# Kernel tuning notes

Measured on AMD Instinct MI355X. Metric: run time of the kernel, lower is better.

Reference implementation:

```python
import jax, jax.numpy as jnp
import numpy as np

NUM_ROUTES = 8
TEMPERATURE = 0.1
NEG_INF = -1e9
EPS = 1e-12  # F.normalize eps


def _l2_normalize(t):
    n = jnp.sqrt(jnp.sum(t * t, axis=-1, keepdims=True))
    return t / jnp.maximum(n, EPS)


def setup_inputs() -> dict:
    key = jax.random.key(0)
    ks = jax.random.split(key, 7)
    B, P1, D = 4, 2049, 1024
    s = 1.0 / np.sqrt(D)
    return {
        "x": jax.random.normal(ks[0], (B, P1, D), jnp.float32),
        "Wq": jax.random.normal(ks[1], (D, D), jnp.float32) * s,
        "bq": jax.random.normal(ks[2], (D,), jnp.float32) * 0.01,
        "Wk": jax.random.normal(ks[3], (D, D), jnp.float32) * s,
        "bk": jax.random.normal(ks[4], (D,), jnp.float32) * 0.01,
        "Wv": jax.random.normal(ks[5], (D, D), jnp.float32) * s,
        "bv": jax.random.normal(ks[6], (D,), jnp.float32) * 0.01,
    }


def reference(x, Wq, bq, Wk, bk, Wv, bv):
    x = x[:, 1:, :]  # skip_first=True
    B, P, D = x.shape
    q = _l2_normalize(x @ Wq.T + bq)
    k = _l2_normalize(x @ Wk.T + bk)
    v = x @ Wv.T + bv
    scores = jnp.einsum('bpd,bqd->bpq', q, k)  # [B,P,P]
    diag = jnp.eye(P, dtype=bool)
    scores = jnp.where(diag[None], NEG_INF, scores)
    topk_scores, routes = jax.lax.top_k(scores / TEMPERATURE, NUM_ROUTES)  # [B,P,K]
    weights = jax.nn.softmax(topk_scores, axis=-1)
    b_idx = jnp.arange(B)[:, None, None]
    v_gathered = v[b_idx, routes]  # [B,P,K,D]
    features = jnp.einsum('bpk,bpkd->bpd', weights, v_gathered)
    return routes, weights, features
```

## Files before the change

kernel.cpp:

```cpp
#include <hip/hip_runtime.h>
#include <hip/hip_bf16.h>
#include <math.h>

#define TEMP 0.1
#define NC 10

typedef float f4 __attribute__((ext_vector_type(4)));
typedef short s8v __attribute__((ext_vector_type(8)));
typedef int   i4v __attribute__((ext_vector_type(4)));
typedef _Float16 h8v __attribute__((ext_vector_type(8)));

__device__ inline short f2bf(float f) {
    __hip_bfloat16 h = __float2bfloat16(f);
    return *reinterpret_cast<short*>(&h);
}

__device__ __forceinline__ void g2l16(const void* g, void* l) {
    __builtin_amdgcn_global_load_lds(
        (const __attribute__((address_space(1))) void*)g,
        (__attribute__((address_space(3))) void*)l, 16, 0, 0);
}

__global__ __launch_bounds__(256) void prep_w(
    const float* __restrict__ Wq, const float* __restrict__ Wk,
    const float* __restrict__ Wv,
    signed char* __restrict__ Wql, signed char* __restrict__ Wkl,
    double* __restrict__ wqsc, double* __restrict__ wksc,
    short* __restrict__ Wvh)
{
    const int row = blockIdx.x, tid = threadIdx.x;
    const int which = blockIdx.y;
    if (which == 2) {
        const float4 v = ((const float4*)(Wv + (size_t)row * 1024))[tid];
        __align__(8) short h[4] = {f2bf(v.x), f2bf(v.y), f2bf(v.z), f2bf(v.w)};
        *(short4*)&Wvh[(size_t)row * 1024 + tid * 4] = *(short4*)h;
        return;
    }
    const float* src = which ? Wk : Wq;
    signed char* limbs = which ? Wkl : Wql;
    double* scale = which ? wksc : wqsc;
    const long plane_stride = 1024L * 1024;

    const float4 v = ((const float4*)(src + (size_t)row * 1024))[tid];
    float m = fmaxf(fmaxf(fabsf(v.x), fabsf(v.y)), fmaxf(fabsf(v.z), fabsf(v.w)));
#pragma unroll
    for (int off = 32; off > 0; off >>= 1) m = fmaxf(m, __shfl_down(m, off));
    __shared__ float wmax[4];
    __shared__ int ssig;
    if ((tid & 63) == 0) wmax[tid >> 6] = m;
    __syncthreads();
    if (tid == 0) {
        float rm = fmaxf(fmaxf(wmax[0], wmax[1]), fmaxf(wmax[2], wmax[3]));
        int sig = (rm > 0.f) ? (29 - ilogbf(rm)) : 0;
        ssig = sig;
        scale[row] = ldexp(1.0, -sig);
    }
    __syncthreads();
    const double s2 = ldexp(1.0, ssig);
    float xs[4] = {v.x, v.y, v.z, v.w};
    signed char out[4][4];
#pragma unroll
    for (int e = 0; e < 4; ++e) {
        long X = __double2ll_rn((double)xs[e] * s2);
#pragma unroll
        for (int l = 0; l < 3; ++l) {
            int d = (int)(((X + 128) & 255) - 128);
            out[l][e] = (signed char)d;
            X = (X - d) >> 8;
        }
        out[3][e] = (signed char)X;
    }
#pragma unroll
    for (int l = 0; l < 4; ++l)
        *(char4*)&limbs[(size_t)l * plane_stride + (size_t)row * 1024 + tid * 4] =
            *(char4*)&out[l][0];
}

__global__ __launch_bounds__(256) void prep_x(
    const float* __restrict__ src, signed char* __restrict__ limbs,
    long plane_stride, double* __restrict__ scale,
    short* __restrict__ hi)
{
    const int row = blockIdx.x, tid = threadIdx.x;
    const float4 v = ((const float4*)(src + (size_t)row * 1024))[tid];
    float m = fmaxf(fmaxf(fabsf(v.x), fabsf(v.y)), fmaxf(fabsf(v.z), fabsf(v.w)));
#pragma unroll
    for (int off = 32; off > 0; off >>= 1) m = fmaxf(m, __shfl_down(m, off));
    __shared__ float wmax[4];
    __shared__ int ssig;
    if ((tid & 63) == 0) wmax[tid >> 6] = m;
    __syncthreads();
    if (tid == 0) {
        float rm = fmaxf(fmaxf(wmax[0], wmax[1]), fmaxf(wmax[2], wmax[3]));
        int sig = (rm > 0.f) ? (29 - ilogbf(rm)) : 0;
        ssig = sig;
        scale[row] = ldexp(1.0, -sig);
    }
    __syncthreads();
    const double s2 = ldexp(1.0, ssig);
    float xs[4] = {v.x, v.y, v.z, v.w};
    signed char out[4][4];
    __align__(8) short h[4];
#pragma unroll
    for (int e = 0; e < 4; ++e) {
        long X = __double2ll_rn((double)xs[e] * s2);
#pragma unroll
        for (int lmb = 0; lmb < 3; ++lmb) {
            int d = (int)(((X + 128) & 255) - 128);
            out[lmb][e] = (signed char)d;
            X = (X - d) >> 8;
        }
        out[3][e] = (signed char)X;
        h[e] = f2bf(xs[e]);
    }
#pragma unroll
    for (int lmb = 0; lmb < 4; ++lmb)
        *(char4*)&limbs[(size_t)lmb * plane_stride + (size_t)row * 1024 + tid * 4] =
            *(char4*)&out[lmb][0];
    *(short4*)&hi[(size_t)row * 1024 + tid * 4] = *(short4*)h;
}

__global__ __launch_bounds__(256, 2) void gemm_i8qk(
    const signed char* __restrict__ Xl,
    const signed char* __restrict__ Wql,
    const signed char* __restrict__ Wkl,
    const double* __restrict__ xsc,
    const double* __restrict__ wqsc, const double* __restrict__ wksc,
    const float* __restrict__ bq, const float* __restrict__ bk,
    float* __restrict__ Qf, float* __restrict__ Kf)
{
    const int K = 1024, N = 1024;
    const long MK = 2048L * 1024, NK = 1024L * 1024;

    __shared__ __align__(16) signed char Asm[4][64][64];
    __shared__ __align__(16) signed char Bqm[4][64][64];
    __shared__ __align__(16) signed char Bkm[4][64][64];

    const int tid  = threadIdx.x;
    const int lane = tid & 63, wave = tid >> 6;
    const int wm = wave >> 1, wn = wave & 1;
    const int quad = lane >> 4, l16 = lane & 15;
    const int m0 = blockIdx.y * 64, n0 = blockIdx.x * 64;

    const int srow = tid >> 2;
    const int cswz = ((tid & 3) ^ ((srow >> 1) & 3));
    const signed char* ap  = Xl  + (size_t)(m0 + srow) * K + cswz * 16;
    const signed char* bqp = Wql + (size_t)(n0 + srow) * K + cswz * 16;
    const signed char* bkp = Wkl + (size_t)(n0 + srow) * K + cswz * 16;

    signed char* aw  = (signed char*)Asm + (wave << 10);
    signed char* bqw = (signed char*)Bqm + (wave << 10);
    signed char* bkw = (signed char*)Bkm + (wave << 10);

    i4v accq[4][2][2] = {};
    i4v acck[4][2][2] = {};

    const int R0  = wm * 32 + l16;
    const int R1  = wm * 32 + 16 + l16;
    const int c0  = (quad ^ ((R0 >> 1) & 3)) * 16;
    const int c1  = (quad ^ ((R1 >> 1) & 3)) * 16;
    const int Rn0 = wn * 32 + l16;
    const int Rn1 = wn * 32 + 16 + l16;
    const int cn0 = (quad ^ ((Rn0 >> 1) & 3)) * 16;
    const int cn1 = (quad ^ ((Rn1 >> 1) & 3)) * 16;

    for (int k0 = 0; k0 < K; k0 += 64) {
        __syncthreads();
#pragma unroll
        for (int l = 0; l < 4; ++l) {
            g2l16(ap  + l * MK + k0, aw  + l * 4096);
            g2l16(bqp + l * NK + k0, bqw + l * 4096);
            g2l16(bkp + l * NK + k0, bkw + l * 4096);
        }
        __syncthreads();

        i4v aF0[4], aF1[4];
#pragma unroll
        for (int i = 0; i < 4; ++i) {
            aF0[i] = *(const i4v*)&Asm[i][R0][c0];
            aF1[i] = *(const i4v*)&Asm[i][R1][c1];
        }

#pragma unroll
        for (int j = 0; j < 4; ++j) {
            i4v bq0 = *(const i4v*)&Bqm[j][Rn0][cn0];
            i4v bq1 = *(const i4v*)&Bqm[j][Rn1][cn1];
            i4v bk0 = *(const i4v*)&Bkm[j][Rn0][cn0];
            i4v bk1 = *(const i4v*)&Bkm[j][Rn1][cn1];
#pragma unroll
            for (int i = 0; i < 4; ++i) {
                if (i + j < 3) continue;
                const int s = i + j - 3;
                accq[s][0][0] = __builtin_amdgcn_mfma_i32_16x16x64_i8(aF0[i], bq0, accq[s][0][0], 0, 0, 0);
                accq[s][0][1] = __builtin_amdgcn_mfma_i32_16x16x64_i8(aF0[i], bq1, accq[s][0][1], 0, 0, 0);
                accq[s][1][0] = __builtin_amdgcn_mfma_i32_16x16x64_i8(aF1[i], bq0, accq[s][1][0], 0, 0, 0);
                accq[s][1][1] = __builtin_amdgcn_mfma_i32_16x16x64_i8(aF1[i], bq1, accq[s][1][1], 0, 0, 0);
                acck[s][0][0] = __builtin_amdgcn_mfma_i32_16x16x64_i8(aF0[i], bk0, acck[s][0][0], 0, 0, 0);
                acck[s][0][1] = __builtin_amdgcn_mfma_i32_16x16x64_i8(aF0[i], bk1, acck[s][0][1], 0, 0, 0);
                acck[s][1][0] = __builtin_amdgcn_mfma_i32_16x16x64_i8(aF1[i], bk0, acck[s][1][0], 0, 0, 0);
                acck[s][1][1] = __builtin_amdgcn_mfma_i32_16x16x64_i8(aF1[i], bk1, acck[s][1][1], 0, 0, 0);
            }
        }
    }

    const double wt0 = ldexp(1.0, 24), wt1 = ldexp(1.0, 32);
    const double wt2 = ldexp(1.0, 40), wt3 = ldexp(1.0, 48);
#pragma unroll
    for (int mt = 0; mt < 2; ++mt)
#pragma unroll
        for (int nt = 0; nt < 2; ++nt)
#pragma unroll
            for (int r = 0; r < 4; ++r) {
                int row = m0 + wm * 32 + mt * 16 + quad * 4 + r;
                int col = n0 + wn * 32 + nt * 16 + l16;
                const double xr = xsc[row];
                double dq = wt0 * (double)accq[0][mt][nt][r]
                          + wt1 * (double)accq[1][mt][nt][r]
                          + wt2 * (double)accq[2][mt][nt][r]
                          + wt3 * (double)accq[3][mt][nt][r];
                Qf[(size_t)row * N + col] =
                    (float)(dq * xr * wqsc[col] + (double)bq[col]);
                double dk = wt0 * (double)acck[0][mt][nt][r]
                          + wt1 * (double)acck[1][mt][nt][r]
                          + wt2 * (double)acck[2][mt][nt][r]
                          + wt3 * (double)acck[3][mt][nt][r];
                Kf[(size_t)row * N + col] =
                    (float)(dk * xr * wksc[col] + (double)bk[col]);
            }
}

__global__ __launch_bounds__(256, 4) void gemm_v64(
    const short* __restrict__ Ahp, const short* __restrict__ Bhp,
    const float* __restrict__ bias, float* __restrict__ C)
{
    const int K = 1024, N = 1024;
    __shared__ __align__(16) short Ah[64][32];
    __shared__ __align__(16) short Bh[64][32];

    const int tid = threadIdx.x, lane = tid & 63, wave = tid >> 6;
    const int wm = wave >> 1, wn = wave & 1;
    const int quad = lane >> 4, l16 = lane & 15;
    const int m0 = blockIdx.y * 64, n0 = blockIdx.x * 64;
    const int srow = tid >> 2;
    const int cswz = ((tid & 3) ^ ((srow >> 1) & 3));
    const char* ap = (const char*)(Ahp + (size_t)(m0 + srow) * K) + cswz * 16;
    const char* bp = (const char*)(Bhp + (size_t)(n0 + srow) * K) + cswz * 16;
    char* aw = (char*)Ah + (wave << 10);
    char* bw = (char*)Bh + (wave << 10);

    f4 acc[2][2] = {};
    for (int k0 = 0; k0 < K; k0 += 32) {
        __syncthreads();
        g2l16(ap + 2 * k0, aw);
        g2l16(bp + 2 * k0, bw);
        __syncthreads();

        s8v af[2], bf[2];
#pragma unroll
        for (int t = 0; t < 2; ++t) {
            const int Ra = wm * 32 + t * 16 + l16;
            const int Rb = wn * 32 + t * 16 + l16;
            af[t] = *(const s8v*)((const char*)Ah + Ra * 64 + ((quad ^ ((Ra >> 1) & 3)) << 4));
            bf[t] = *(const s8v*)((const char*)Bh + Rb * 64 + ((quad ^ ((Rb >> 1) & 3)) << 4));
        }
#pragma unroll
        for (int mt = 0; mt < 2; ++mt)
#pragma unroll
            for (int nt = 0; nt < 2; ++nt)
                acc[mt][nt] = __builtin_amdgcn_mfma_f32_16x16x32_bf16(
                    af[mt], bf[nt], acc[mt][nt], 0, 0, 0);
    }
#pragma unroll
    for (int mt = 0; mt < 2; ++mt)
#pragma unroll
        for (int nt = 0; nt < 2; ++nt)
#pragma unroll
            for (int r = 0; r < 4; ++r) {
                int row = m0 + wm * 32 + mt * 16 + quad * 4 + r;
                int col = n0 + wn * 32 + nt * 16 + l16;
                C[(size_t)row * N + col] = acc[mt][nt][r] + bias[col];
            }
}

__global__ __launch_bounds__(256, 4) void gemm_score(
    const short* __restrict__ Qh, const short* __restrict__ Kh,
    float* __restrict__ C)
{
    const int K = 1024, N = 2048;
    __shared__ __align__(16) short As[64][32];
    __shared__ __align__(16) short Bs[64][32];
    const int tid = threadIdx.x, lane = tid & 63, wave = tid >> 6;
    const int wm = wave >> 1, wn = wave & 1;
    const int quad = lane >> 4, l16 = lane & 15;
    const int m0 = blockIdx.y * 64, n0 = blockIdx.x * 64;
    const int srow = tid >> 2;
    const int cswz = ((tid & 3) ^ ((srow >> 1) & 3));
    const char* ap = (const char*)(Qh + (size_t)(m0 + srow) * K) + cswz * 16;
    const char* bp = (const char*)(Kh + (size_t)(n0 + srow) * K) + cswz * 16;
    char* aw = (char*)As + (wave << 10);
    char* bw = (char*)Bs + (wave << 10);

    f4 acc[2][2] = {};
    for (int k0 = 0; k0 < K; k0 += 32) {
        __syncthreads();
        g2l16(ap + 2 * k0, aw);
        g2l16(bp + 2 * k0, bw);
        __syncthreads();

        h8v af[2], bf[2];
#pragma unroll
        for (int t = 0; t < 2; ++t) {
            const int Ra = wm * 32 + t * 16 + l16;
            const int Rb = wn * 32 + t * 16 + l16;
            af[t] = *(const h8v*)((const char*)As + Ra * 64 + ((quad ^ ((Ra >> 1) & 3)) << 4));
            bf[t] = *(const h8v*)((const char*)Bs + Rb * 64 + ((quad ^ ((Rb >> 1) & 3)) << 4));
        }
#pragma unroll
        for (int mt = 0; mt < 2; ++mt)
#pragma unroll
            for (int nt = 0; nt < 2; ++nt)
                acc[mt][nt] = __builtin_amdgcn_mfma_f32_16x16x32_f16(
                    af[mt], bf[nt], acc[mt][nt], 0, 0, 0);
    }
#pragma unroll
    for (int mt = 0; mt < 2; ++mt)
#pragma unroll
        for (int nt = 0; nt < 2; ++nt)
#pragma unroll
            for (int r = 0; r < 4; ++r) {
                int row = m0 + wm * 32 + mt * 16 + quad * 4 + r;
                int col = n0 + wn * 32 + nt * 16 + l16;
                C[(size_t)row * N + col] = acc[mt][nt][r];
            }
}

__global__ __launch_bounds__(256) void l2norm_f32h16(
    float* __restrict__ fq, float* __restrict__ fk,
    short* __restrict__ hq, short* __restrict__ hk)
{
    float* f = blockIdx.y ? fk : fq;
    short* h = blockIdx.y ? hk : hq;
    const int row = blockIdx.x;
    const int tid = threadIdx.x;
    float4* p4 = (float4*)(f + (size_t)row * 1024);
    float4 v = p4[tid];
    double s = (double)v.x * v.x + (double)v.y * v.y
             + (double)v.z * v.z + (double)v.w * v.w;
#pragma unroll
    for (int off = 32; off > 0; off >>= 1) s += __shfl_down(s, off);
    __shared__ double ws[5];
    if ((tid & 63) == 0) ws[tid >> 6] = s;
    __syncthreads();
    if (tid == 0) ws[4] = fmax(sqrt(ws[0] + ws[1] + ws[2] + ws[3]), 1e-12);
    __syncthreads();
    const double inv = 1.0 / ws[4];
    float o0 = (float)(v.x * inv), o1 = (float)(v.y * inv);
    float o2 = (float)(v.z * inv), o3 = (float)(v.w * inv);
    float4 o = make_float4(o0, o1, o2, o3);
    p4[tid] = o;
    __align__(8) _Float16 hv[4] = {(_Float16)o0, (_Float16)o1,
                                   (_Float16)o2, (_Float16)o3};
    *(short4*)&h[(size_t)row * 1024 + tid * 4] = *(short4*)hv;
}

__global__ __launch_bounds__(256) void topk_route(
    const float*  __restrict__ S,
    const float*  __restrict__ Qf,
    const float*  __restrict__ Kf,
    const float*  __restrict__ Vf,
    float* __restrict__ routes_out,
    float* __restrict__ weights_out,
    float* __restrict__ feat_out,
    int batch)
{
    const int P = 2048, D = 1024;
    __shared__ float  qrow[1024];
    __shared__ float  cval[4 * NC];
    __shared__ int    cidx[4 * NC];
    __shared__ int    sel[NC];
    __shared__ double cscore[NC];
    __shared__ int    topi_s[8];
    __shared__ float  wts[8];

    const int p = blockIdx.x;
    const int tid = threadIdx.x;
    const int lane = tid & 63, wave = tid >> 6;

    const float4* sr4 = (const float4*)(S + (size_t)p * P);
    const float4 s0 = sr4[tid];
    const float4 s1 = sr4[tid + 256];
    ((float4*)qrow)[tid] = ((const float4*)(Qf + (size_t)p * D))[tid];

    float v[8] = {s0.x, s0.y, s0.z, s0.w, s1.x, s1.y, s1.z, s1.w};
    int   ji[8];
#pragma unroll
    for (int e = 0; e < 8; ++e) {
        ji[e] = (e < 4) ? (4 * tid + e) : (1024 + 4 * tid + (e - 4));
        if (ji[e] == p) v[e] = -1e30f;
    }

    float lv = v[0]; int li = ji[0];
#pragma unroll
    for (int e = 1; e < 8; ++e)
        if (v[e] > lv) { lv = v[e]; li = ji[e]; }

    float cv_ = -INFINITY; int ci_ = 0x7fffffff;
#pragma unroll 1
    for (int it = 0; it < NC; ++it) {
        float bv = lv; int bi = li;
#pragma unroll
        for (int off = 32; off > 0; off >>= 1) {
            float ov = __shfl_xor(bv, off);
            int   oi = __shfl_xor(bi, off);
            if (ov > bv || (ov == bv && oi < bi)) { bv = ov; bi = oi; }
        }
        if (lane == it) { cv_ = bv; ci_ = bi; }
#pragma unroll
        for (int e = 0; e < 8; ++e)
            if (ji[e] == bi) v[e] = -INFINITY;
        lv = v[0]; li = ji[0];
#pragma unroll
        for (int e = 1; e < 8; ++e)
            if (v[e] > lv) { lv = v[e]; li = ji[e]; }
    }
    if (lane < NC) { cval[wave * NC + lane] = cv_; cidx[wave * NC + lane] = ci_; }
    __syncthreads();

    if (wave == 0) {
        float mv = (lane < 4 * NC) ? cval[lane] : -INFINITY;
        int   mi = (lane < 4 * NC) ? cidx[lane] : 0x7fffffff;
        int rank = 0;
#pragma unroll 1
        for (int j = 0; j < 4 * NC; ++j) {
            float vj = __shfl(mv, j);
            int   ij = __shfl(mi, j);
            rank += (vj > mv || (vj == mv && ij < mi)) ? 1 : 0;
        }
        if (lane < 4 * NC && rank < NC) sel[rank] = mi;
    }
    __syncthreads();

    float pfv[8];
#pragma unroll
    for (int c = 0; c < 8; ++c)
        pfv[c] = Vf[(size_t)sel[c] * D + tid * 4];

    {
        const float* k0r = Kf + (size_t)sel[wave] * D;
        const float* k1r = Kf + (size_t)sel[wave + 4] * D;
        const float* k2r = Kf + (size_t)sel[8 + (wave & 1)] * D;
        double a0 = 0.0, a1 = 0.0, a2 = 0.0;
#pragma unroll 4
        for (int j = 0; j < 8; ++j) {
            const int e = lane * 2 + j * 128;
            const float2 q2 = *(const float2*)&qrow[e];
            const float2 kA = *(const float2*)&k0r[e];
            const float2 kB = *(const float2*)&k1r[e];
            const float2 kC = *(const float2*)&k2r[e];
            a0 = fma((double)q2.x, (double)kA.x, fma((double)q2.y, (double)kA.y, a0));
            a1 = fma((double)q2.x, (double)kB.x, fma((double)q2.y, (double)kB.y, a1));
            a2 = fma((double)q2.x, (double)kC.x, fma((double)q2.y, (double)kC.y, a2));
        }
#pragma unroll
        for (int off = 32; off > 0; off >>= 1) {
            a0 += __shfl_xor(a0, off);
            a1 += __shfl_xor(a1, off);
            a2 += __shfl_xor(a2, off);
        }
        if (lane == 0) {
            cscore[wave]     = a0;
            cscore[wave + 4] = a1;
            if (wave < 2) cscore[8 + wave] = a2;
        }
    }

    {
        float pf = 0.f;
#pragma unroll
        for (int c = 0; c < 8; ++c) pf += pfv[c];
        asm volatile("" :: "v"(pf));
    }
    __syncthreads();

    if (wave == 0) {
        double sc_ = (lane < NC) ? cscore[lane] : -1.0e308;
        int    id_ = (lane < NC) ? sel[lane]    : 0x7fffffff;
        int rank = 0;
#pragma unroll
        for (int j = 0; j < NC; ++j) {
            double vj = __shfl(sc_, j);
            int    ij = __shfl(id_, j);
            rank += (vj > sc_ || (vj == sc_ && ij < id_)) ? 1 : 0;
        }
        double mm = sc_;
#pragma unroll
        for (int off = 32; off > 0; off >>= 1) mm = fmax(mm, __shfl_xor(mm, off));
        double e = (rank < 8 && lane < NC) ? exp((sc_ - mm) / TEMP) : 0.0;
        double sum = e;
#pragma unroll
        for (int off = 32; off > 0; off >>= 1) sum += __shfl_xor(sum, off);
        if (rank < 8 && lane < NC) {
            float wk = (float)(e / sum);
            wts[rank] = wk; topi_s[rank] = id_;
            const size_t row = (size_t)batch * P + p;
            routes_out[row * 8 + rank]  = (float)id_;
            weights_out[row * 8 + rank] = wk;
        }
    }
    __syncthreads();

    float4 a = {0.f, 0.f, 0.f, 0.f};
#pragma unroll
    for (int k = 0; k < 8; ++k) {
        const float4 v4 = ((const float4*)(Vf + (size_t)topi_s[k] * D))[tid];
        float wk = wts[k];
        a.x = fmaf(wk, v4.x, a.x);
        a.y = fmaf(wk, v4.y, a.y);
        a.z = fmaf(wk, v4.z, a.z);
        a.w = fmaf(wk, v4.w, a.w);
    }
    ((float4*)(feat_out + ((size_t)batch * P + p) * D))[tid] = a;
}

extern "C" void kernel_launch(void* const* d_in, const int* in_sizes, int n_in,
                              void* d_out, int out_size, void* d_ws, size_t ws_size,
                              hipStream_t stream)
{
    const float* x  = (const float*)d_in[0];
    const float* Wq = (const float*)d_in[1];
    const float* bq = (const float*)d_in[2];
    const float* Wk = (const float*)d_in[3];
    const float* bk = (const float*)d_in[4];
    const float* Wv = (const float*)d_in[5];
    const float* bv = (const float*)d_in[6];

    const int B = 4, P = 2048, D = 1024;
    const size_t PD = (size_t)P * D;
    const size_t DD = (size_t)D * D;

    float*  Qf   = (float*)d_ws;
    float*  Kf   = Qf + PD;
    double* xsc  = (double*)(Kf + PD);
    double* wqsc = xsc + 2048;
    double* wksc = wqsc + 1024;
    short*  Qh   = (short*)(wksc + 1024);
    short*  Kh   = Qh + PD;
    short*  xh   = Kh + PD;
    short*  Wvh  = xh + PD;
    float*  Vf   = (float*)(Wvh + DD);
    float*  Sf   = Vf + PD;
    signed char* Xl  = (signed char*)(Sf + (size_t)P * P);
    signed char* Wql = Xl + 4 * PD;
    signed char* Wkl = Wql + 4 * DD;

    float* out     = (float*)d_out;
    float* routes  = out;
    float* weights = out + (size_t)B * P * 8;
    float* feat    = out + (size_t)B * P * 16;

    dim3 blk(256);
    prep_w<<<dim3(1024, 3), blk, 0, stream>>>(Wq, Wk, Wv, Wql, Wkl, wqsc, wksc, Wvh);

    for (int b = 0; b < B; ++b) {
        const float* xb = x + ((size_t)b * 2049 + 1) * D;
        prep_x<<<dim3(P), blk, 0, stream>>>(xb, Xl, (long)PD, xsc, xh);
        gemm_i8qk<<<dim3(16, 32), blk, 0, stream>>>(Xl, Wql, Wkl, xsc, wqsc, wksc,
                                                    bq, bk, Qf, Kf);
        gemm_v64<<<dim3(16, 32), blk, 0, stream>>>(xh, Wvh, bv, Vf);
        l2norm_f32h16<<<dim3(P, 2), blk, 0, stream>>>(Qf, Kf, Qh, Kh);
        gemm_score<<<dim3(32, 32), blk, 0, stream>>>(Qh, Kh, Sf);
        topk_route<<<dim3(P), blk, 0, stream>>>(Sf, Qf, Kf, Vf, routes, weights, feat, b);
    }
}
```

Measured before the change: 599.7 us.

## Fuse Q/K and V projection GEMMs and overlap next-batch prep with top-k

Merges the int8 Q/K GEMM and the bf16 V GEMM into one launch, with alternating blocks taking each job. The topk kernel now also runs the next batch's prep_x in odd blocks, so the prep stage overlaps with routing. This cuts kernel launches and fills the tails between small grids. The cost is that the fused GEMM kernel declares the shared memory for both paths, which may reduce occupancy.

```diff
diff --git a/kernel.cpp b/kernel.cpp
--- a/kernel.cpp
+++ b/kernel.cpp
@@ -76,28 +76,28 @@
             *(char4*)&out[l][0];
 }
 
-__global__ __launch_bounds__(256) void prep_x(
+
+struct PrepSm { float wmax[4]; int ssig; };
+
+__device__ __forceinline__ void prepx_body(
+    PrepSm* sm, int row, int tid,
     const float* __restrict__ src, signed char* __restrict__ limbs,
-    long plane_stride, double* __restrict__ scale,
-    short* __restrict__ hi)
-{
-    const int row = blockIdx.x, tid = threadIdx.x;
+    long plane_stride, double* __restrict__ scale, short* __restrict__ hi)
+{
     const float4 v = ((const float4*)(src + (size_t)row * 1024))[tid];
     float m = fmaxf(fmaxf(fabsf(v.x), fabsf(v.y)), fmaxf(fabsf(v.z), fabsf(v.w)));
 #pragma unroll
     for (int off = 32; off > 0; off >>= 1) m = fmaxf(m, __shfl_down(m, off));
-    __shared__ float wmax[4];
-    __shared__ int ssig;
-    if ((tid & 63) == 0) wmax[tid >> 6] = m;
+    if ((tid & 63) == 0) sm->wmax[tid >> 6] = m;
     __syncthreads();
     if (tid == 0) {
-        float rm = fmaxf(fmaxf(wmax[0], wmax[1]), fmaxf(wmax[2], wmax[3]));
+        float rm = fmaxf(fmaxf(sm->wmax[0], sm->wmax[1]), fmaxf(sm->wmax[2], sm->wmax[3]));
         int sig = (rm > 0.f) ? (29 - ilogbf(rm)) : 0;
-        ssig = sig;
+        sm->ssig = sig;
         scale[row] = ldexp(1.0, -sig);
     }
     __syncthreads();
-    const double s2 = ldexp(1.0, ssig);
+    const double s2 = ldexp(1.0, sm->ssig);
     float xs[4] = {v.x, v.y, v.z, v.w};
     signed char out[4][4];
     __align__(8) short h[4];
@@ -120,27 +120,24 @@
     *(short4*)&hi[(size_t)row * 1024 + tid * 4] = *(short4*)h;
 }
 
-__global__ __launch_bounds__(256, 2) void gemm_i8qk(
+__device__ __forceinline__ void i8qk_body(
+    signed char* As, signed char* Bq, signed char* Bk,
+    int xt, int yt, int tid,
     const signed char* __restrict__ Xl,
     const signed char* __restrict__ Wql,
     const signed char* __restrict__ Wkl,
     const double* __restrict__ xsc,
     const double* __restrict__ wqsc, const double* __restrict__ wksc,
-    const float* __restrict__ bq, const float* __restrict__ bk,
+    const float* __restrict__ bqb, const float* __restrict__ bkb,
     float* __restrict__ Qf, float* __restrict__ Kf)
 {
     const int K = 1024, N = 1024;
     const long MK = 2048L * 1024, NK = 1024L * 1024;
 
-    __shared__ __align__(16) signed char Asm[4][64][64];
-    __shared__ __align__(16) signed char Bqm[4][64][64];
-    __shared__ __align__(16) signed char Bkm[4][64][64];
-
-    const int tid  = threadIdx.x;
     const int lane = tid & 63, wave = tid >> 6;
     const int wm = wave >> 1, wn = wave & 1;
     const int quad = lane >> 4, l16 = lane & 15;
-    const int m0 = blockIdx.y * 64, n0 = blockIdx.x * 64;
+    const int m0 = yt * 64, n0 = xt * 64;
 
     const int srow = tid >> 2;
     const int cswz = ((tid & 3) ^ ((srow >> 1) & 3));
@@ -148,9 +145,9 @@
     const signed char* bqp = Wql + (size_t)(n0 + srow) * K + cswz * 16;
     const signed char* bkp = Wkl + (size_t)(n0 + srow) * K + cswz * 16;
 
-    signed char* aw  = (signed char*)Asm + (wave << 10);
-    signed char* bqw = (signed char*)Bqm + (wave << 10);
-    signed char* bkw = (signed char*)Bkm + (wave << 10);
+    signed char* aw  = As + (wave << 10);
+    signed char* bqw = Bq + (wave << 10);
+    signed char* bkw = Bk + (wave << 10);
 
     i4v accq[4][2][2] = {};
     i4v acck[4][2][2] = {};
@@ -177,16 +174,16 @@
         i4v aF0[4], aF1[4];
 #pragma unroll
         for (int i = 0; i < 4; ++i) {
-            aF0[i] = *(const i4v*)&Asm[i][R0][c0];
-            aF1[i] = *(const i4v*)&Asm[i][R1][c1];
+            aF0[i] = *(const i4v*)(As + i * 4096 + R0 * 64 + c0);
+            aF1[i] = *(const i4v*)(As + i * 4096 + R1 * 64 + c1);
         }
 
 #pragma unroll
         for (int j = 0; j < 4; ++j) {
-            i4v bq0 = *(const i4v*)&Bqm[j][Rn0][cn0];
-            i4v bq1 = *(const i4v*)&Bqm[j][Rn1][cn1];
-            i4v bk0 = *(const i4v*)&Bkm[j][Rn0][cn0];
-            i4v bk1 = *(const i4v*)&Bkm[j][Rn1][cn1];
+            i4v bq0 = *(const i4v*)(Bq + j * 4096 + Rn0 * 64 + cn0);
+            i4v bq1 = *(const i4v*)(Bq + j * 4096 + Rn1 * 64 + cn1);
+            i4v bk0 = *(const i4v*)(Bk + j * 4096 + Rn0 * 64 + cn0);
+            i4v bk1 = *(const i4v*)(Bk + j * 4096 + Rn1 * 64 + cn1);
 #pragma unroll
             for (int i = 0; i < 4; ++i) {
                 if (i + j < 3) continue;
@@ -219,34 +216,32 @@
                           + wt2 * (double)accq[2][mt][nt][r]
                           + wt3 * (double)accq[3][mt][nt][r];
                 Qf[(size_t)row * N + col] =
-                    (float)(dq * xr * wqsc[col] + (double)bq[col]);
+                    (float)(dq * xr * wqsc[col] + (double)bqb[col]);
                 double dk = wt0 * (double)acck[0][mt][nt][r]
                           + wt1 * (double)acck[1][mt][nt][r]
                           + wt2 * (double)acck[2][mt][nt][r]
                           + wt3 * (double)acck[3][mt][nt][r];
                 Kf[(size_t)row * N + col] =
-                    (float)(dk * xr * wksc[col] + (double)bk[col]);
+                    (float)(dk * xr * wksc[col] + (double)bkb[col]);
             }
 }
 
-__global__ __launch_bounds__(256, 4) void gemm_v64(
+__device__ __forceinline__ void v64_body(
+    char* Ahc, char* Bhc, int xt, int yt, int tid,
     const short* __restrict__ Ahp, const short* __restrict__ Bhp,
     const float* __restrict__ bias, float* __restrict__ C)
 {
     const int K = 1024, N = 1024;
-    __shared__ __align__(16) short Ah[64][32];
-    __shared__ __align__(16) short Bh[64][32];
-
-    const int tid = threadIdx.x, lane = tid & 63, wave = tid >> 6;
+    const int lane = tid & 63, wave = tid >> 6;
     const int wm = wave >> 1, wn = wave & 1;
     const int quad = lane >> 4, l16 = lane & 15;
-    const int m0 = blockIdx.y * 64, n0 = blockIdx.x * 64;
+    const int m0 = yt * 64, n0 = xt * 64;
     const int srow = tid >> 2;
     const int cswz = ((tid & 3) ^ ((srow >> 1) & 3));
     const char* ap = (const char*)(Ahp + (size_t)(m0 + srow) * K) + cswz * 16;
     const char* bp = (const char*)(Bhp + (size_t)(n0 + srow) * K) + cswz * 16;
-    char* aw = (char*)Ah + (wave << 10);
-    char* bw = (char*)Bh + (wave << 10);
+    char* aw = Ahc + (wave << 10);
+    char* bw = Bhc + (wave << 10);
 
     f4 acc[2][2] = {};
     for (int k0 = 0; k0 < K; k0 += 32) {
@@ -260,8 +255,8 @@
         for (int t = 0; t < 2; ++t) {
             const int Ra = wm * 32 + t * 16 + l16;
             const int Rb = wn * 32 + t * 16 + l16;
-            af[t] = *(const s8v*)((const char*)Ah + Ra * 64 + ((quad ^ ((Ra >> 1) & 3)) << 4));
-            bf[t] = *(const s8v*)((const char*)Bh + Rb * 64 + ((quad ^ ((Rb >> 1) & 3)) << 4));
+            af[t] = *(const s8v*)(Ahc + Ra * 64 + ((quad ^ ((Ra >> 1) & 3)) << 4));
+            bf[t] = *(const s8v*)(Bhc + Rb * 64 + ((quad ^ ((Rb >> 1) & 3)) << 4));
         }
 #pragma unroll
         for (int mt = 0; mt < 2; ++mt)
@@ -280,6 +275,237 @@
                 int col = n0 + wn * 32 + nt * 16 + l16;
                 C[(size_t)row * N + col] = acc[mt][nt][r] + bias[col];
             }
+}
+
+struct TopkSm {
+    float  qrow[1024];
+    float  cval[4 * NC];
+    int    cidx[4 * NC];
+    int    sel[NC];
+    double cscore[NC];
+    int    topi_s[8];
+    float  wts[8];
+};
+
+__device__ __forceinline__ void topk_body(
+    TopkSm* sm, int p, int tid,
+    const float* __restrict__ S,
+    const float* __restrict__ Qf,
+    const float* __restrict__ Kf,
+    const float* __restrict__ Vf,
+    float* __restrict__ routes_out,
+    float* __restrict__ weights_out,
+    float* __restrict__ feat_out,
+    int batch)
+{
+    const int P = 2048, D = 1024;
+    const int lane = tid & 63, wave = tid >> 6;
+
+    const float4* sr4 = (const float4*)(S + (size_t)p * P);
+    const float4 s0 = sr4[tid];
+    const float4 s1 = sr4[tid + 256];
+    ((float4*)sm->qrow)[tid] = ((const float4*)(Qf + (size_t)p * D))[tid];
+
+    float v[8] = {s0.x, s0.y, s0.z, s0.w, s1.x, s1.y, s1.z, s1.w};
+    int   ji[8];
+#pragma unroll
+    for (int e = 0; e < 8; ++e) {
+        ji[e] = (e < 4) ? (4 * tid + e) : (1024 + 4 * tid + (e - 4));
+        if (ji[e] == p) v[e] = -1e30f;
+    }
+
+    float lv = v[0]; int li = ji[0];
+#pragma unroll
+    for (int e = 1; e < 8; ++e)
+        if (v[e] > lv) { lv = v[e]; li = ji[e]; }
+
+    float cv_ = -INFINITY; int ci_ = 0x7fffffff;
+#pragma unroll 1
+    for (int it = 0; it < NC; ++it) {
+        float bv = lv; int bi = li;
+#pragma unroll
+        for (int off = 32; off > 0; off >>= 1) {
+            float ov = __shfl_xor(bv, off);
+            int   oi = __shfl_xor(bi, off);
+            if (ov > bv || (ov == bv && oi < bi)) { bv = ov; bi = oi; }
+        }
+        if (lane == it) { cv_ = bv; ci_ = bi; }
+#pragma unroll
+        for (int e = 0; e < 8; ++e)
+            if (ji[e] == bi) v[e] = -INFINITY;
+        lv = v[0]; li = ji[0];
+#pragma unroll
+        for (int e = 1; e < 8; ++e)
+            if (v[e] > lv) { lv = v[e]; li = ji[e]; }
+    }
+    if (lane < NC) { sm->cval[wave * NC + lane] = cv_; sm->cidx[wave * NC + lane] = ci_; }
+    __syncthreads();
+
+    if (wave == 0) {
+        float mv = (lane < 4 * NC) ? sm->cval[lane] : -INFINITY;
+        int   mi = (lane < 4 * NC) ? sm->cidx[lane] : 0x7fffffff;
+        int rank = 0;
+#pragma unroll 1
+        for (int j = 0; j < 4 * NC; ++j) {
+            float vj = __shfl(mv, j);
+            int   ij = __shfl(mi, j);
+            rank += (vj > mv || (vj == mv && ij < mi)) ? 1 : 0;
+        }
+        if (lane < 4 * NC && rank < NC) sm->sel[rank] = mi;
+    }
+    __syncthreads();
+
+    float pfv[8];
+#pragma unroll
+    for (int c = 0; c < 8; ++c)
+        pfv[c] = Vf[(size_t)sm->sel[c] * D + tid * 4];
+
+    {
+        const float* k0r = Kf + (size_t)sm->sel[wave] * D;
+        const float* k1r = Kf + (size_t)sm->sel[wave + 4] * D;
+        const float* k2r = Kf + (size_t)sm->sel[8 + (wave & 1)] * D;
+        double a0 = 0.0, a1 = 0.0, a2 = 0.0;
+#pragma unroll 4
+        for (int j = 0; j < 8; ++j) {
+            const int e = lane * 2 + j * 128;
+            const float2 q2 = *(const float2*)&sm->qrow[e];
+            const float2 kA = *(const float2*)&k0r[e];
+            const float2 kB = *(const float2*)&k1r[e];
+            const float2 kC = *(const float2*)&k2r[e];
+            a0 = fma((double)q2.x, (double)kA.x, fma((double)q2.y, (double)kA.y, a0));
+            a1 = fma((double)q2.x, (double)kB.x, fma((double)q2.y, (double)kB.y, a1));
+            a2 = fma((double)q2.x, (double)kC.x, fma((double)q2.y, (double)kC.y, a2));
+        }
+#pragma unroll
+        for (int off = 32; off > 0; off >>= 1) {
+            a0 += __shfl_xor(a0, off);
+            a1 += __shfl_xor(a1, off);
+            a2 += __shfl_xor(a2, off);
+        }
+        if (lane == 0) {
+            sm->cscore[wave]     = a0;
+            sm->cscore[wave + 4] = a1;
+            if (wave < 2) sm->cscore[8 + wave] = a2;
+        }
+    }
+
+    {
+        float pf = 0.f;
+#pragma unroll
+        for (int c = 0; c < 8; ++c) pf += pfv[c];
+        asm volatile("" :: "v"(pf));
+    }
+    __syncthreads();
+
+    if (wave == 0) {
+        double sc_ = (lane < NC) ? sm->cscore[lane] : -1.0e308;
+        int    id_ = (lane < NC) ? sm->sel[lane]    : 0x7fffffff;
+        int rank = 0;
+#pragma unroll
+        for (int j = 0; j < NC; ++j) {
+            double vj = __shfl(sc_, j);
+            int    ij = __shfl(id_, j);
+            rank += (vj > sc_ || (vj == sc_ && ij < id_)) ? 1 : 0;
+        }
+        double mm = sc_;
+#pragma unroll
+        for (int off = 32; off > 0; off >>= 1) mm = fmax(mm, __shfl_xor(mm, off));
+        double e = (rank < 8 && lane < NC) ? exp((sc_ - mm) / TEMP) : 0.0;
+        double sum = e;
+#pragma unroll
+        for (int off = 32; off > 0; off >>= 1) sum += __shfl_xor(sum, off);
+        if (rank < 8 && lane < NC) {
+            float wk = (float)(e / sum);
+            sm->wts[rank] = wk; sm->topi_s[rank] = id_;
+            const size_t row = (size_t)batch * P + p;
+            routes_out[row * 8 + rank]  = (float)id_;
+            weights_out[row * 8 + rank] = wk;
+        }
+    }
+    __syncthreads();
+
+    float4 a = {0.f, 0.f, 0.f, 0.f};
+#pragma unroll
+    for (int k = 0; k < 8; ++k) {
+        const float4 v4 = ((const float4*)(Vf + (size_t)sm->topi_s[k] * D))[tid];
+        float wk = sm->wts[k];
+        a.x = fmaf(wk, v4.x, a.x);
+        a.y = fmaf(wk, v4.y, a.y);
+        a.z = fmaf(wk, v4.z, a.z);
+        a.w = fmaf(wk, v4.w, a.w);
+    }
+    ((float4*)(feat_out + ((size_t)batch * P + p) * D))[tid] = a;
+}
+
+
+__global__ __launch_bounds__(256, 2) void gemm_qkv(
+    const signed char* __restrict__ Xl,
+    const signed char* __restrict__ Wql,
+    const signed char* __restrict__ Wkl,
+    const double* __restrict__ xsc,
+    const double* __restrict__ wqsc, const double* __restrict__ wksc,
+    const float* __restrict__ bq, const float* __restrict__ bk,
+    float* __restrict__ Qf, float* __restrict__ Kf,
+    const short* __restrict__ xh, const short* __restrict__ Wvh,
+    const float* __restrict__ bv, float* __restrict__ Vf)
+{
+    __shared__ __align__(16) signed char iA[4 * 64 * 64];
+    __shared__ __align__(16) signed char iBq[4 * 64 * 64];
+    __shared__ __align__(16) signed char iBk[4 * 64 * 64];
+    __shared__ __align__(16) char vA[64 * 64];
+    __shared__ __align__(16) char vB[64 * 64];
+    const int xt = blockIdx.x >> 1, yt = blockIdx.y, tid = threadIdx.x;
+    if (blockIdx.x & 1)
+        v64_body(vA, vB, xt, yt, tid, xh, Wvh, bv, Vf);
+    else
+        i8qk_body(iA, iBq, iBk, xt, yt, tid, Xl, Wql, Wkl,
+                  xsc, wqsc, wksc, bq, bk, Qf, Kf);
+}
+
+__global__ __launch_bounds__(256) void prep_x(
+    const float* __restrict__ src, signed char* __restrict__ limbs,
+    long plane_stride, double* __restrict__ scale,
+    short* __restrict__ hi)
+{
+    __shared__ PrepSm psm;
+    prepx_body(&psm, blockIdx.x, threadIdx.x, src, limbs, plane_stride, scale, hi);
+}
+
+__global__ __launch_bounds__(256) void topk_prepx(
+    const float* __restrict__ S,
+    const float* __restrict__ Qf,
+    const float* __restrict__ Kf,
+    const float* __restrict__ Vf,
+    float* __restrict__ routes_out,
+    float* __restrict__ weights_out,
+    float* __restrict__ feat_out,
+    int batch,
+    const float* __restrict__ xnext, signed char* __restrict__ Xl,
+    long plane_stride, double* __restrict__ xsc, short* __restrict__ xh)
+{
+    __shared__ TopkSm tsm;
+    __shared__ PrepSm psm;
+    const int tid = threadIdx.x;
+    if (blockIdx.x & 1)
+        prepx_body(&psm, blockIdx.x >> 1, tid, xnext, Xl, plane_stride, xsc, xh);
+    else
+        topk_body(&tsm, blockIdx.x >> 1, tid, S, Qf, Kf, Vf,
+                  routes_out, weights_out, feat_out, batch);
+}
+
+__global__ __launch_bounds__(256) void topk_route(
+    const float* __restrict__ S,
+    const float* __restrict__ Qf,
+    const float* __restrict__ Kf,
+    const float* __restrict__ Vf,
+    float* __restrict__ routes_out,
+    float* __restrict__ weights_out,
+    float* __restrict__ feat_out,
+    int batch)
+{
+    __shared__ TopkSm tsm;
+    topk_body(&tsm, blockIdx.x, threadIdx.x, S, Qf, Kf, Vf,
+              routes_out, weights_out, feat_out, batch);
 }
 
 __global__ __launch_bounds__(256, 4) void gemm_score(
@@ -361,165 +587,6 @@
     __align__(8) _Float16 hv[4] = {(_Float16)o0, (_Float16)o1,
                                    (_Float16)o2, (_Float16)o3};
     *(short4*)&h[(size_t)row * 1024 + tid * 4] = *(short4*)hv;
-}
-
-__global__ __launch_bounds__(256) void topk_route(
-    const float*  __restrict__ S,
-    const float*  __restrict__ Qf,
-    const float*  __restrict__ Kf,
-    const float*  __restrict__ Vf,
-    float* __restrict__ routes_out,
-    float* __restrict__ weights_out,
-    float* __restrict__ feat_out,
-    int batch)
-{
-    const int P = 2048, D = 1024;
-    __shared__ float  qrow[1024];
-    __shared__ float  cval[4 * NC];
-    __shared__ int    cidx[4 * NC];
-    __shared__ int    sel[NC];
-    __shared__ double cscore[NC];
-    __shared__ int    topi_s[8];
-    __shared__ float  wts[8];
-
-    const int p = blockIdx.x;
-    const int tid = threadIdx.x;
-    const int lane = tid & 63, wave = tid >> 6;
-
-    const float4* sr4 = (const float4*)(S + (size_t)p * P);
-    const float4 s0 = sr4[tid];
-    const float4 s1 = sr4[tid + 256];
-    ((float4*)qrow)[tid] = ((const float4*)(Qf + (size_t)p * D))[tid];
-
-    float v[8] = {s0.x, s0.y, s0.z, s0.w, s1.x, s1.y, s1.z, s1.w};
-    int   ji[8];
-#pragma unroll
-    for (int e = 0; e < 8; ++e) {
-        ji[e] = (e < 4) ? (4 * tid + e) : (1024 + 4 * tid + (e - 4));
-        if (ji[e] == p) v[e] = -1e30f;
-    }
-
-    float lv = v[0]; int li = ji[0];
-#pragma unroll
-    for (int e = 1; e < 8; ++e)
-        if (v[e] > lv) { lv = v[e]; li = ji[e]; }
-
-    float cv_ = -INFINITY; int ci_ = 0x7fffffff;
-#pragma unroll 1
-    for (int it = 0; it < NC; ++it) {
-        float bv = lv; int bi = li;
-#pragma unroll
-        for (int off = 32; off > 0; off >>= 1) {
-            float ov = __shfl_xor(bv, off);
-            int   oi = __shfl_xor(bi, off);
-            if (ov > bv || (ov == bv && oi < bi)) { bv = ov; bi = oi; }
-        }
-        if (lane == it) { cv_ = bv; ci_ = bi; }
-#pragma unroll
-        for (int e = 0; e < 8; ++e)
-            if (ji[e] == bi) v[e] = -INFINITY;
-        lv = v[0]; li = ji[0];
-#pragma unroll
-        for (int e = 1; e < 8; ++e)
-            if (v[e] > lv) { lv = v[e]; li = ji[e]; }
-    }
-    if (lane < NC) { cval[wave * NC + lane] = cv_; cidx[wave * NC + lane] = ci_; }
-    __syncthreads();
-
-    if (wave == 0) {
-        float mv = (lane < 4 * NC) ? cval[lane] : -INFINITY;
-        int   mi = (lane < 4 * NC) ? cidx[lane] : 0x7fffffff;
-        int rank = 0;
-#pragma unroll 1
-        for (int j = 0; j < 4 * NC; ++j) {
-            float vj = __shfl(mv, j);
-            int   ij = __shfl(mi, j);
-            rank += (vj > mv || (vj == mv && ij < mi)) ? 1 : 0;
-        }
-        if (lane < 4 * NC && rank < NC) sel[rank] = mi;
-    }
-    __syncthreads();
-
-    float pfv[8];
-#pragma unroll
-    for (int c = 0; c < 8; ++c)
-        pfv[c] = Vf[(size_t)sel[c] * D + tid * 4];
-
-    {
-        const float* k0r = Kf + (size_t)sel[wave] * D;
-        const float* k1r = Kf + (size_t)sel[wave + 4] * D;
-        const float* k2r = Kf + (size_t)sel[8 + (wave & 1)] * D;
-        double a0 = 0.0, a1 = 0.0, a2 = 0.0;
-#pragma unroll 4
-        for (int j = 0; j < 8; ++j) {
-            const int e = lane * 2 + j * 128;
-            const float2 q2 = *(const float2*)&qrow[e];
-            const float2 kA = *(const float2*)&k0r[e];
-            const float2 kB = *(const float2*)&k1r[e];
-            const float2 kC = *(const float2*)&k2r[e];
-            a0 = fma((double)q2.x, (double)kA.x, fma((double)q2.y, (double)kA.y, a0));
-            a1 = fma((double)q2.x, (double)kB.x, fma((double)q2.y, (double)kB.y, a1));
-            a2 = fma((double)q2.x, (double)kC.x, fma((double)q2.y, (double)kC.y, a2));
-        }
-#pragma unroll
-        for (int off = 32; off > 0; off >>= 1) {
-            a0 += __shfl_xor(a0, off);
-            a1 += __shfl_xor(a1, off);
-            a2 += __shfl_xor(a2, off);
-        }
-        if (lane == 0) {
-            cscore[wave]     = a0;
-            cscore[wave + 4] = a1;
-            if (wave < 2) cscore[8 + wave] = a2;
-        }
-    }
-
-    {
-        float pf = 0.f;
-#pragma unroll
-        for (int c = 0; c < 8; ++c) pf += pfv[c];
-        asm volatile("" :: "v"(pf));
-    }
-    __syncthreads();
-
-    if (wave == 0) {
-        double sc_ = (lane < NC) ? cscore[lane] : -1.0e308;
-        int    id_ = (lane < NC) ? sel[lane]    : 0x7fffffff;
-        int rank = 0;
-#pragma unroll
-        for (int j = 0; j < NC; ++j) {
-            double vj = __shfl(sc_, j);
-            int    ij = __shfl(id_, j);
-            rank += (vj > sc_ || (vj == sc_ && ij < id_)) ? 1 : 0;
-        }
-        double mm = sc_;
-#pragma unroll
-        for (int off = 32; off > 0; off >>= 1) mm = fmax(mm, __shfl_xor(mm, off));
-        double e = (rank < 8 && lane < NC) ? exp((sc_ - mm) / TEMP) : 0.0;
-        double sum = e;
-#pragma unroll
-        for (int off = 32; off > 0; off >>= 1) sum += __shfl_xor(sum, off);
-        if (rank < 8 && lane < NC) {
-            float wk = (float)(e / sum);
-            wts[rank] = wk; topi_s[rank] = id_;
-            const size_t row = (size_t)batch * P + p;
-            routes_out[row * 8 + rank]  = (float)id_;
-            weights_out[row * 8 + rank] = wk;
-        }
-    }
-    __syncthreads();
-
-    float4 a = {0.f, 0.f, 0.f, 0.f};
-#pragma unroll
-    for (int k = 0; k < 8; ++k) {
-        const float4 v4 = ((const float4*)(Vf + (size_t)topi_s[k] * D))[tid];
-        float wk = wts[k];
-        a.x = fmaf(wk, v4.x, a.x);
-        a.y = fmaf(wk, v4.y, a.y);
-        a.z = fmaf(wk, v4.z, a.z);
-        a.w = fmaf(wk, v4.w, a.w);
-    }
-    ((float4*)(feat_out + ((size_t)batch * P + p) * D))[tid] = a;
 }
 
 extern "C" void kernel_launch(void* const* d_in, const int* in_sizes, int n_in,
@@ -560,15 +627,21 @@
 
     dim3 blk(256);
     prep_w<<<dim3(1024, 3), blk, 0, stream>>>(Wq, Wk, Wv, Wql, Wkl, wqsc, wksc, Wvh);
+    prep_x<<<dim3(P), blk, 0, stream>>>(x + D, Xl, (long)PD, xsc, xh);
 
     for (int b = 0; b < B; ++b) {
-        const float* xb = x + ((size_t)b * 2049 + 1) * D;
-        prep_x<<<dim3(P), blk, 0, stream>>>(xb, Xl, (long)PD, xsc, xh);
-        gemm_i8qk<<<dim3(16, 32), blk, 0, stream>>>(Xl, Wql, Wkl, xsc, wqsc, wksc,
-                                                    bq, bk, Qf, Kf);
-        gemm_v64<<<dim3(16, 32), blk, 0, stream>>>(xh, Wvh, bv, Vf);
+        gemm_qkv<<<dim3(32, 32), blk, 0, stream>>>(Xl, Wql, Wkl, xsc, wqsc, wksc,
+                                                   bq, bk, Qf, Kf, xh, Wvh, bv, Vf);
         l2norm_f32h16<<<dim3(P, 2), blk, 0, stream>>>(Qf, Kf, Qh, Kh);
         gemm_score<<<dim3(32, 32), blk, 0, stream>>>(Qh, Kh, Sf);
-        topk_route<<<dim3(P), blk, 0, stream>>>(Sf, Qf, Kf, Vf, routes, weights, feat, b);
-    }
-}
+        if (b < B - 1) {
+            const float* xn = x + ((size_t)(b + 1) * 2049 + 1) * D;
+            topk_prepx<<<dim3(2 * P), blk, 0, stream>>>(Sf, Qf, Kf, Vf,
+                                                        routes, weights, feat, b,
+                                                        xn, Xl, (long)PD, xsc, xh);
+        } else {
+            topk_route<<<dim3(P), blk, 0, stream>>>(Sf, Qf, Kf, Vf,
+                                                    routes, weights, feat, b);
+        }
+    }
+}
```

Measured after the change: 706.7 us. 1.18x slower.
